# Performance work log

Measured on AMD Instinct MI355X. Metric: run time of the kernel, lower is better.

Reference implementation:

```python
import jax, jax.numpy as jnp
import numpy as np

STRIDE = 1
PAD = 3  # kernel_size // 2


def _dwconv(x, w, stride, pad):
    # x: [N,C,H,W], w: [C,1,k,k], depthwise (feature_group_count = C)
    C = x.shape[1]
    return jax.lax.conv_general_dilated(
        x, w,
        window_strides=(stride, stride),
        padding=[(pad, pad), (pad, pad)],
        dimension_numbers=("NCHW", "OIHW", "NCHW"),
        feature_group_count=C,
    )


def setup_inputs() -> dict:
    key = jax.random.key(0)
    k1, k2 = jax.random.split(key)
    x = jax.random.normal(k1, (16, 384, 64, 64), dtype=jnp.float32)
    # kaiming_normal_(mode='fan_out', nonlinearity='relu'): std = sqrt(2 / fan_out)
    k_sz = 7
    fan_out = 1 * k_sz * k_sz  # out_channels_per_group * k * k for grouped conv
    std = np.sqrt(2.0 / fan_out).astype(np.float32)
    weight = jax.random.normal(k2, (384, 1, k_sz, k_sz), dtype=jnp.float32) * std
    return {"x": x, "weight": weight}


def reference(x, weight):
    # (conv(x,w0)+conv(x,w90)+conv(x,w180)+conv(x,w270))/4 == conv(x, mean of rotated kernels)
    # (convolution is linear in the kernel; bias=None). Same math, one conv launch.
    w_sym = (weight
             + jnp.rot90(weight, k=1, axes=(2, 3))
             + jnp.rot90(weight, k=2, axes=(2, 3))
             + jnp.rot90(weight, k=3, axes=(2, 3))) * 0.25
    return _dwconv(x, w_sym, STRIDE, PAD)
```

## Files before the change

kernel.cpp:

```cpp
#include <hip/hip_runtime.h>
#include <cstddef>


#define BLOCK 256
#define TS 68
#define TROWS 70
#define TILE_F (4 + TROWS * TS)

constexpr int canon_of(int k) {
    const int i = k / 7, j = k % 7;
    const int a = i * 7 + j;
    const int b = j * 7 + (6 - i);
    const int c = (6 - i) * 7 + (6 - j);
    const int d = (6 - j) * 7 + i;
    int m = a;
    if (b < m) m = b;
    if (c < m) m = c;
    if (d < m) m = d;
    return m;
}
struct Tab { int cidx[49]; };
constexpr Tab build_tab() {
    Tab t{};
    int u = 0;
    for (int k = 0; k < 49; ++k)
        if (canon_of(k) == k) { t.cidx[k] = u; ++u; }
    for (int k = 0; k < 49; ++k) t.cidx[k] = t.cidx[canon_of(k)];
    return t;
}
constexpr Tab TAB = build_tab();

__global__ __launch_bounds__(BLOCK, 8) void dwconv7_sym_kernel(
    const float* __restrict__ x, const float* __restrict__ w,
    float* __restrict__ out, int C)
{
    __shared__ __align__(16) float tile[TILE_F];
    __shared__ float wsym[49];
    float4* const tile4 = (float4*)tile;

    const int plane = blockIdx.x;
    const int c = plane % C;
    const int tid = threadIdx.x;

    const float4* __restrict__ xp4 = (const float4*)(x + (size_t)plane * 4096);
    float4 gv[4];
    #pragma unroll
    for (int k = 0; k < 4; ++k)
        gv[k] = xp4[k * BLOCK + tid];

    if (tid < 52) tile4[tid] = make_float4(0.f, 0.f, 0.f, 0.f);
    if (tid >= 64 && tid < 115) tile4[1140 + (tid - 64)] = make_float4(0.f, 0.f, 0.f, 0.f);

    if (tid < 49) {
        const int i = tid / 7;
        const int j = tid - i * 7;
        const float* wc = w + c * 49;
        wsym[tid] = 0.25f * (wc[i * 7 + j]
                           + wc[j * 7 + (6 - i)]
                           + wc[(6 - i) * 7 + (6 - j)]
                           + wc[(6 - j) * 7 + i]);
    }

    #pragma unroll
    for (int k = 0; k < 4; ++k) {
        const int g = k * BLOCK + tid;
        const int grow = g >> 4;
        const int gcol = g & 15;
        tile4[1 + (grow + 3) * 17 + gcol] = gv[k];
    }
    __syncthreads();

    float wu[13];
    #pragma unroll
    for (int k = 0; k < 49; ++k)
        if (canon_of(k) == k) wu[TAB.cidx[k]] = wsym[k];

    const int cg = tid & 15;
    const int S  = tid >> 4;
    const int x0 = 4 * cg;

    float acc[4][4];
    #pragma unroll
    for (int t = 0; t < 4; ++t)
        #pragma unroll
        for (int d = 0; d < 4; ++d) acc[t][d] = 0.f;

    #pragma unroll
    for (int ro = 0; ro < 10; ++ro) {
        const int row = 4 * S + ro;
        const float4* p4 = (const float4*)(tile + row * TS + x0);
        float4 a = p4[0], b = p4[1], cc = p4[2];
        if (cg == 0)  { a.x = 0.f; a.y = 0.f; a.z = 0.f; a.w = 0.f; }
        if (cg == 15) { cc.x = 0.f; cc.y = 0.f; cc.z = 0.f; }
        const float r[12] = {a.x, a.y, a.z, a.w, b.x, b.y, b.z, b.w,
                             cc.x, cc.y, cc.z, cc.w};
        #pragma unroll
        for (int t = 0; t < 4; ++t) {
            if (t <= ro && ro <= t + 6) {
                const int i = ro - t;
                #pragma unroll
                for (int d = 0; d < 4; ++d)
                    #pragma unroll
                    for (int j = 0; j < 7; ++j)
                        acc[t][d] += r[d + j + 1] * wu[TAB.cidx[i * 7 + j]];
            }
        }
    }

    float4* __restrict__ op4 = (float4*)(out + (size_t)plane * 4096);
    #pragma unroll
    for (int t = 0; t < 4; ++t) {
        float4 v;
        v.x = acc[t][0]; v.y = acc[t][1]; v.z = acc[t][2]; v.w = acc[t][3];
        op4[(4 * S + t) * 16 + cg] = v;
    }
}

extern "C" void kernel_launch(void* const* d_in, const int* in_sizes, int n_in,
                              void* d_out, int out_size, void* d_ws, size_t ws_size,
                              hipStream_t stream) {
    const float* x = (const float*)d_in[0];
    const float* w = (const float*)d_in[1];
    float* out = (float*)d_out;

    const int planes = in_sizes[0] / 4096;
    const int C = in_sizes[1] / 49;

    dwconv7_sym_kernel<<<dim3(planes), dim3(BLOCK), 0, stream>>>(x, w, out, C);
}
```

Baseline: 184.9 us.

## Read input directly from global memory instead of staging through LDS tile

Drops the shared-memory tile and its barrier; each thread now loads its 10 rows × 3 float4 neighbourhood straight from global memory (via L1/L2), with clamped row indices and zero masking for padding. Symmetrised weights are computed per thread from global memory rather than via a shared array, and the launch-bounds occupancy hint drops from 8 to 6. This removes the LDS staging and sync cost but multiplies global/cache load traffic by roughly 7.5x and relies on cache hits.

```diff
diff --git a/kernel.cpp b/kernel.cpp
--- a/kernel.cpp
+++ b/kernel.cpp
@@ -3,9 +3,6 @@
 
 
 #define BLOCK 256
-#define TS 68
-#define TROWS 70
-#define TILE_F (4 + TROWS * TS)
 
 constexpr int canon_of(int k) {
     const int i = k / 7, j = k % 7;
@@ -30,54 +27,31 @@
 }
 constexpr Tab TAB = build_tab();
 
-__global__ __launch_bounds__(BLOCK, 8) void dwconv7_sym_kernel(
+__global__ __launch_bounds__(BLOCK, 6) void dwconv7_sym_kernel(
     const float* __restrict__ x, const float* __restrict__ w,
     float* __restrict__ out, int C)
 {
-    __shared__ __align__(16) float tile[TILE_F];
-    __shared__ float wsym[49];
-    float4* const tile4 = (float4*)tile;
-
     const int plane = blockIdx.x;
     const int c = plane % C;
     const int tid = threadIdx.x;
 
-    const float4* __restrict__ xp4 = (const float4*)(x + (size_t)plane * 4096);
-    float4 gv[4];
-    #pragma unroll
-    for (int k = 0; k < 4; ++k)
-        gv[k] = xp4[k * BLOCK + tid];
-
-    if (tid < 52) tile4[tid] = make_float4(0.f, 0.f, 0.f, 0.f);
-    if (tid >= 64 && tid < 115) tile4[1140 + (tid - 64)] = make_float4(0.f, 0.f, 0.f, 0.f);
-
-    if (tid < 49) {
-        const int i = tid / 7;
-        const int j = tid - i * 7;
-        const float* wc = w + c * 49;
-        wsym[tid] = 0.25f * (wc[i * 7 + j]
-                           + wc[j * 7 + (6 - i)]
-                           + wc[(6 - i) * 7 + (6 - j)]
-                           + wc[(6 - j) * 7 + i]);
-    }
-
-    #pragma unroll
-    for (int k = 0; k < 4; ++k) {
-        const int g = k * BLOCK + tid;
-        const int grow = g >> 4;
-        const int gcol = g & 15;
-        tile4[1 + (grow + 3) * 17 + gcol] = gv[k];
-    }
-    __syncthreads();
-
+    const float* __restrict__ wc = w + c * 49;
     float wu[13];
     #pragma unroll
-    for (int k = 0; k < 49; ++k)
-        if (canon_of(k) == k) wu[TAB.cidx[k]] = wsym[k];
+    for (int k = 0; k < 49; ++k) {
+        if (canon_of(k) == k) {
+            const int i = k / 7, j = k % 7;
+            wu[TAB.cidx[k]] = 0.25f * (wc[i * 7 + j]
+                                     + wc[j * 7 + (6 - i)]
+                                     + wc[(6 - i) * 7 + (6 - j)]
+                                     + wc[(6 - j) * 7 + i]);
+        }
+    }
 
     const int cg = tid & 15;
     const int S  = tid >> 4;
     const int x0 = 4 * cg;
+    const float* __restrict__ xp = x + (size_t)plane * 4096;
 
     float acc[4][4];
     #pragma unroll
@@ -87,9 +61,17 @@
 
     #pragma unroll
     for (int ro = 0; ro < 10; ++ro) {
-        const int row = 4 * S + ro;
-        const float4* p4 = (const float4*)(tile + row * TS + x0);
-        float4 a = p4[0], b = p4[1], cc = p4[2];
+        const int row = 4 * S + ro - 3;
+        const int rr  = (row < 0) ? 0 : (row > 63 ? 63 : row);
+        const float4* p = (const float4*)(xp + rr * 64 + x0);
+        const float4* pa = (cg == 0)  ? p : (p - 1);
+        const float4* pc = (cg == 15) ? p : (p + 1);
+        float4 a = *pa, b = *p, cc = *pc;
+        if ((unsigned)row >= 64u) {
+            a.x = 0.f; a.y = 0.f; a.z = 0.f; a.w = 0.f;
+            b.x = 0.f; b.y = 0.f; b.z = 0.f; b.w = 0.f;
+            cc.x = 0.f; cc.y = 0.f; cc.z = 0.f; cc.w = 0.f;
+        }
         if (cg == 0)  { a.x = 0.f; a.y = 0.f; a.z = 0.f; a.w = 0.f; }
         if (cg == 15) { cc.x = 0.f; cc.y = 0.f; cc.z = 0.f; }
         const float r[12] = {a.x, a.y, a.z, a.w, b.x, b.y, b.z, b.w,
```

Result: slower. 503.3 us (+172.2%).
